# Performance work log

Hardware: AMD Instinct MI355X
Metric: run time of the kernel (lower is better)

## Reference

```python
import jax, jax.numpy as jnp
import numpy as np

B, H, W, C = 16, 64, 64, 256
DIRECTIONS = [(0, -1), (1, -1), (1, 0), (1, 1), (0, 1), (-1, 1), (-1, 0), (-1, -1)]


def _shift(g, dx, dy):
    # zero-padded shift matching the torch _shift_grid semantics:
    # result[:, max(0,dy):H+min(0,dy), max(0,dx):W+min(0,dx)] = g[src slices]
    _, h, w, _ = g.shape
    padded = jnp.pad(g, ((0, 0), (max(0, dy), max(0, -dy)), (max(0, dx), max(0, -dx)), (0, 0)))
    return padded[:, max(0, -dy):max(0, -dy) + h, max(0, -dx):max(0, -dx) + w, :]


def setup_inputs() -> dict:
    key = jax.random.key(0)
    k1, k2, k3, k4 = jax.random.split(key, 4)
    grid_embedding = jax.random.normal(k1, (B, H, W, C), dtype=jnp.float32)
    Wd = jax.random.normal(k2, (8, C, C), dtype=jnp.float32) * 0.01  # per-direction weights
    Wc = jax.random.normal(k3, (C, 8 * C), dtype=jnp.float32) * 0.02  # Linear weight [out, in]
    bc = jax.random.normal(k4, (C,), dtype=jnp.float32) * 0.02
    return {"grid_embedding": grid_embedding, "Wd": Wd, "Wc": Wc, "bc": bc}


def reference(grid_embedding, Wd, Wc, bc):
    # stack the 8 zero-padded shifted copies: [8, B, H, W, C]
    shifted = jnp.stack([_shift(grid_embedding, dx, dy) for (dx, dy) in DIRECTIONS], axis=0)
    # per-direction channel matmul: [B, H, W, 8, C] (d-major over last two dims matches torch.cat order)
    proc = jnp.einsum('dbhwc,dce->bhwde', shifted, Wd)
    combined = proc.reshape(grid_embedding.shape[0], grid_embedding.shape[1], grid_embedding.shape[2], -1)
    # nn.Linear: y = x @ W.T + b
    return combined @ Wc.T + bc
```

## Files before the change

kernel.cpp:

```cpp
#include <hip/hip_runtime.h>


typedef unsigned short u16;
typedef unsigned int u32;
typedef __attribute__((ext_vector_type(8))) short bf16x8;
typedef __attribute__((ext_vector_type(4))) float f32x4;

#define GP_BYTES 35684352

__device__ __forceinline__ u16 f2bf(float f) {
  u32 u = __float_as_uint(f);
  u32 r = u + 0x7fffu + ((u >> 16) & 1u);
  return (u16)(r >> 16);
}
__device__ __forceinline__ u32 pack2(float a, float b) {
  return (u32)f2bf(a) | ((u32)f2bf(b) << 16);
}

__global__ __launch_bounds__(256) void pad_convert(const float* __restrict__ g,
                                                   u16* __restrict__ gp) {
  int id = blockIdx.x * 256 + threadIdx.x;
  if (id >= 2230272) return;
  int c8 = id & 31;
  int t = id >> 5;
  int xx = t % 66;
  int s = t / 66;
  int yy = s % 66;
  int b  = s / 66;
  u32 o0 = 0, o1 = 0, o2 = 0, o3 = 0;
  if (yy != 0 && yy != 65 && xx != 0 && xx != 65) {
    const float* src = g + ((((b << 6) + yy - 1) << 6) + xx - 1) * 256 + (c8 << 3);
    float4 fa = *(const float4*)src;
    float4 fb = *(const float4*)(src + 4);
    o0 = pack2(fa.x, fa.y);
    o1 = pack2(fa.z, fa.w);
    o2 = pack2(fb.x, fb.y);
    o3 = pack2(fb.z, fb.w);
  }
  uint4 v; v.x = o0; v.y = o1; v.z = o2; v.w = o3;
  *(uint4*)(gp + (size_t)id * 8) = v;
}

__global__ __launch_bounds__(256) void build_mt(const float* __restrict__ Wd,
                                                const float* __restrict__ Wc,
                                                u16* __restrict__ Bf) {
  __shared__ __align__(16) u16 As[128 * 32];
  __shared__ __align__(16) u16 Bs[128 * 32];
  const int bid = blockIdx.x;
  const int n0    = (bid & 1) << 7;
  const int mblk  = bid >> 1;
  const int d     = mblk >> 1;
  const int chalf = (mblk & 1) << 7;
  const int tid  = threadIdx.x;
  const int lane = tid & 63, wid = tid >> 6;
  const int wm = (wid >> 1) << 6, wn = (wid & 1) << 6;
  const int quad = lane >> 4, r16 = lane & 15;
  const int srow = tid >> 1, hh = tid & 1;
  const int swz  = (srow >> 1) & 3;
  const int ssl  = (quad ^ ((r16 >> 1) & 3)) << 3;
  f32x4 acc[4][4] = {};

  for (int e0 = 0; e0 < 256; e0 += 32) {
    __syncthreads();
    const float* pa = Wd + (size_t)(d * 256 + chalf + srow) * 256 + e0 + hh * 16;
    const float* pb = Wc + (size_t)(n0 + srow) * 2048 + d * 256 + e0 + hh * 16;
#pragma unroll
    for (int i = 0; i < 2; ++i) {
      float4 a0 = *(const float4*)(pa + i * 8);
      float4 a1 = *(const float4*)(pa + i * 8 + 4);
      float4 b0 = *(const float4*)(pb + i * 8);
      float4 b1 = *(const float4*)(pb + i * 8 + 4);
      uint4 va, vb;
      va.x = pack2(a0.x, a0.y); va.y = pack2(a0.z, a0.w);
      va.z = pack2(a1.x, a1.y); va.w = pack2(a1.z, a1.w);
      vb.x = pack2(b0.x, b0.y); vb.y = pack2(b0.z, b0.w);
      vb.z = pack2(b1.x, b1.y); vb.w = pack2(b1.z, b1.w);
      int slot = (2 * hh + i) ^ swz;
      *(uint4*)&As[srow * 32 + slot * 8] = va;
      *(uint4*)&Bs[srow * 32 + slot * 8] = vb;
    }
    __syncthreads();
    bf16x8 bfr[4];
#pragma unroll
    for (int nt = 0; nt < 4; ++nt)
      bfr[nt] = *(const bf16x8*)&Bs[(wn + nt * 16 + r16) * 32 + ssl];
#pragma unroll
    for (int mt = 0; mt < 4; ++mt) {
      bf16x8 af = *(const bf16x8*)&As[(wm + mt * 16 + r16) * 32 + ssl];
#pragma unroll
      for (int nt = 0; nt < 4; ++nt)
        acc[mt][nt] = __builtin_amdgcn_mfma_f32_16x16x32_bf16(af, bfr[nt], acc[mt][nt], 0, 0, 0);
    }
  }
#pragma unroll
  for (int mt = 0; mt < 4; ++mt) {
#pragma unroll
    for (int nt = 0; nt < 4; ++nt) {
      const int o = n0 + wn + nt * 16 + r16;
      f32x4 v = acc[mt][nt];
#pragma unroll
      for (int r = 0; r < 4; ++r) {
        const int c = chalf + wm + mt * 16 + quad * 4 + r;
        const int lane2 = (o & 15) + (((c >> 3) & 3) << 4);
        const size_t idx = ((size_t)((d * 8 + (c >> 5)) * 16 + (o >> 4)) * 512) + lane2 * 8 + (c & 7);
        Bf[idx] = f2bf(v[r]);
      }
    }
  }
}

__constant__ int DOFF[8] = {16896, 16640, -256, -17152, -16896, -16640, 256, 17152};

__device__ __forceinline__ void async16(const u16* g, u16* l) {
  __builtin_amdgcn_global_load_lds((const __attribute__((address_space(1))) u32*)g,
                                   (__attribute__((address_space(3))) u32*)l, 16, 0, 0);
}

__global__ __launch_bounds__(512, 2) void conv_gemm(const u16* __restrict__ gp,
                                                    const u16* __restrict__ Bf,
                                                    const float* __restrict__ bc,
                                                    float* __restrict__ out) {
  __shared__ __align__(16) u16 Asm[4][8192];
  const int bid = blockIdx.x;
  const int id2 = ((bid & 7) << 5) | (bid >> 3);
  const int b   = id2 >> 4;
  const int y0  = (id2 & 15) << 2;

  const int tid  = threadIdx.x;
  const int lane = tid & 63;
  const int wid  = tid >> 6;
  const int wm   = (wid >> 2) << 7;
  const int wn   = (wid & 3) << 6;
  const int quad = lane >> 4;
  const int r16  = lane & 15;

  const int chunk = (tid & 3) ^ ((tid >> 3) & 3);
  const u16* baseA = gp + ((b * 66 + y0 + 1 + (tid >> 8)) * 66 + ((tid >> 2) & 63) + 1) * 256
                        + (chunk << 3);
  const int ldso = tid * 8;

  const u16* baseBf = Bf + ((wn >> 4) << 9) + lane * 8;

  const int ssl = (quad ^ ((r16 >> 1) & 3)) << 3;

  f32x4 acc[8][4] = {};
  bf16x8 Be[4], Bo[4];
  bf16x8 afl[4], afh[4];

  auto issueA = [&](int kt) {
    const int off = DOFF[kt >> 3] + ((kt & 7) << 5);
    async16(baseA + off,         Asm[kt & 3] + ldso);
    async16(baseA + off + 33792, Asm[kt & 3] + 4096 + ldso);
  };
  auto loadB = [&](int kt, bf16x8* dst) {
    const u16* bp = baseBf + (size_t)kt * 8192;
#pragma unroll
    for (int nt = 0; nt < 4; ++nt) dst[nt] = *(const bf16x8*)(bp + nt * 512);
  };
  auto readAh = [&](int kt, bf16x8* af, int h) {
    const u16* Ab = Asm[kt & 3];
#pragma unroll
    for (int mt = 0; mt < 4; ++mt)
      af[mt] = *(const bf16x8*)&Ab[(wm + (h * 4 + mt) * 16 + r16) * 32 + ssl];
  };
  auto mfma_half = [&](const bf16x8* af, const bf16x8* bb, int h) {
    __builtin_amdgcn_s_setprio(1);
#pragma unroll
    for (int mt = 0; mt < 4; ++mt)
#pragma unroll
      for (int nt = 0; nt < 4; ++nt)
        acc[h * 4 + mt][nt] =
            __builtin_amdgcn_mfma_f32_16x16x32_bf16(af[mt], bb[nt], acc[h * 4 + mt][nt], 0, 0, 0);
    __builtin_amdgcn_s_setprio(0);
  };

  auto body = [&](int kt, bf16x8* bu, bool doB, bool doA, int vm) {
    readAh(kt, afh, 1);
    mfma_half(afl, bu, 0);
    readAh(kt + 1, afl, 0);
    mfma_half(afh, bu, 1);
    if (doB) loadB(kt + 2, bu);
    if (doA) issueA(kt + 3);
    if (vm == 6)      asm volatile("s_waitcnt vmcnt(6)" ::: "memory");
    else if (vm == 4) asm volatile("s_waitcnt vmcnt(4)" ::: "memory");
    else              asm volatile("s_waitcnt vmcnt(0)" ::: "memory");
    asm volatile("s_barrier" ::: "memory");
  };

  loadB(0, Be);
  issueA(0);
  issueA(1);
  loadB(1, Bo);
  issueA(2);
  asm volatile("s_waitcnt vmcnt(6)" ::: "memory");
  asm volatile("s_barrier" ::: "memory");
  readAh(0, afl, 0);

  for (int kt = 0; kt < 60; kt += 2) {
    body(kt,     Be, true, true, 6);
    body(kt + 1, Bo, true, true, 6);
  }
  body(60, Be, true,  true,  6);
  body(61, Bo, true,  false, 4);
  body(62, Be, false, false, 0);
  readAh(63, afh, 1);
  mfma_half(afl, Bo, 0);
  mfma_half(afh, Bo, 1);

  const int pbase = (b * 64 + y0) * 64;
#pragma unroll
  for (int nt = 0; nt < 4; ++nt) {
    const int o = wn + nt * 16 + r16;
    const float bias = bc[o];
#pragma unroll
    for (int mt = 0; mt < 8; ++mt) {
      const int pr = pbase + wm + mt * 16 + quad * 4;
      f32x4 v = acc[mt][nt];
#pragma unroll
      for (int r = 0; r < 4; ++r)
        out[(size_t)(pr + r) * 256 + o] = v[r] + bias;
    }
  }
}

extern "C" void kernel_launch(void* const* d_in, const int* in_sizes, int n_in,
                              void* d_out, int out_size, void* d_ws, size_t ws_size,
                              hipStream_t stream) {
  const float* g  = (const float*)d_in[0];
  const float* Wd = (const float*)d_in[1];
  const float* Wc = (const float*)d_in[2];
  const float* bc = (const float*)d_in[3];
  float* out = (float*)d_out;
  u16* gp = (u16*)d_ws;
  u16* Bf = (u16*)((char*)d_ws + GP_BYTES);

  pad_convert<<<8712, 256, 0, stream>>>(g, gp);
  build_mt<<<32, 256, 0, stream>>>(Wd, Wc, Bf);
  conv_gemm<<<256, 512, 0, stream>>>(gp, Bf, bc, out);
}
```

Before: 190.4 us.

## Load padded halo slab once per channel chunk and reuse across all eight directions

Instead of issuing a separate async global-to-LDS copy of the shifted A tile for every (direction, channel-chunk) k-step, each block now loads one swizzled 6x66 padded slab per 32-channel chunk into a triple-buffered LDS ring. The eight directional shifts are taken as row offsets into that slab. This cuts global/L2 traffic for A by about 8x and removes most per-k-step barriers and waits, with a barrier only once per slab. In exchange it uses more LDS (3x12800 bf16), adds extra halo loads, and makes the B-prefetch schedule and vmcnt accounting more intricate.

Result: faster. 181.9 us (-4.5%).

```diff
diff --git a/kernel.cpp b/kernel.cpp
--- a/kernel.cpp
+++ b/kernel.cpp
@@ -109,8 +109,6 @@
   }
 }
 
-__constant__ int DOFF[8] = {16896, 16640, -256, -17152, -16896, -16640, 256, 17152};
-
 __device__ __forceinline__ void async16(const u16* g, u16* l) {
   __builtin_amdgcn_global_load_lds((const __attribute__((address_space(1))) u32*)g,
                                    (__attribute__((address_space(3))) u32*)l, 16, 0, 0);
@@ -120,7 +118,7 @@
                                                     const u16* __restrict__ Bf,
                                                     const float* __restrict__ bc,
                                                     float* __restrict__ out) {
-  __shared__ __align__(16) u16 Asm[4][8192];
+  __shared__ __align__(16) u16 slab[3][12800];
   const int bid = blockIdx.x;
   const int id2 = ((bid & 7) << 5) | (bid >> 3);
   const int b   = id2 >> 4;
@@ -134,34 +132,52 @@
   const int quad = lane >> 4;
   const int r16  = lane & 15;
 
-  const int chunk = (tid & 3) ^ ((tid >> 3) & 3);
-  const u16* baseA = gp + ((b * 66 + y0 + 1 + (tid >> 8)) * 66 + ((tid >> 2) & 63) + 1) * 256
-                        + (chunk << 3);
-  const int ldso = tid * 8;
+  const int i0 = tid, i1 = tid + 512, i2 = tid + 1024, i3 = 1536 + lane;
+  const u16 *p0, *p1, *p2, *p3;
+  {
+    const size_t rowb = (size_t)(b * 66 + y0) * 66;
+    int s, c;
+    s = i0 >> 2; c = (i0 & 3) ^ ((s >> 1) & 3);
+    p0 = gp + (rowb + (s / 66) * 66 + (s % 66)) * 256 + c * 8;
+    s = i1 >> 2; c = (i1 & 3) ^ ((s >> 1) & 3);
+    p1 = gp + (rowb + (s / 66) * 66 + (s % 66)) * 256 + c * 8;
+    s = i2 >> 2; c = (i2 & 3) ^ ((s >> 1) & 3);
+    p2 = gp + (rowb + (s / 66) * 66 + (s % 66)) * 256 + c * 8;
+    s = i3 >> 2; c = (i3 & 3) ^ ((s >> 1) & 3);
+    p3 = gp + (rowb + (s / 66) * 66 + (s % 66)) * 256 + c * 8;
+  }
+  const int l0 = i0 * 8, l1 = i1 * 8, l2 = i2 * 8, l3 = i3 * 8;
 
   const u16* baseBf = Bf + ((wn >> 4) << 9) + lane * 8;
 
-  const int ssl = (quad ^ ((r16 >> 1) & 3)) << 3;
+  const int swm = (wm >> 6) * 66 + r16;
+  const int q8  = quad << 3;
+
+  constexpr int KLO[8] = {133, 132, 66,  0,  1,  2,  68, 134};
+  constexpr int KHI[8] = {199, 198, 132, 66, 67, 68, 134, 200};
+  constexpr int LBO[8] = {2 * 65536, 3 * 65536, 4 * 65536, 5 * 65536,
+                          6 * 65536, 7 * 65536, 8192, 8192 + 65536};
 
   f32x4 acc[8][4] = {};
   bf16x8 Be[4], Bo[4];
   bf16x8 afl[4], afh[4];
 
-  auto issueA = [&](int kt) {
-    const int off = DOFF[kt >> 3] + ((kt & 7) << 5);
-    async16(baseA + off,         Asm[kt & 3] + ldso);
-    async16(baseA + off + 33792, Asm[kt & 3] + 4096 + ldso);
-  };
-  auto loadB = [&](int kt, bf16x8* dst) {
-    const u16* bp = baseBf + (size_t)kt * 8192;
-#pragma unroll
-    for (int nt = 0; nt < 4; ++nt) dst[nt] = *(const bf16x8*)(bp + nt * 512);
-  };
-  auto readAh = [&](int kt, bf16x8* af, int h) {
-    const u16* Ab = Asm[kt & 3];
-#pragma unroll
-    for (int mt = 0; mt < 4; ++mt)
-      af[mt] = *(const bf16x8*)&Ab[(wm + (h * 4 + mt) * 16 + r16) * 32 + ssl];
+  auto issueSlab = [&](u16* dst, int ch) {
+    async16(p0 + ch, dst + l0);
+    async16(p1 + ch, dst + l1);
+    async16(p2 + ch, dst + l2);
+    async16(p3 + ch, dst + l3);
+  };
+  auto loadB = [&](const u16* pB, int off, bf16x8* dst) {
+#pragma unroll
+    for (int nt = 0; nt < 4; ++nt) dst[nt] = *(const bf16x8*)(pB + off + nt * 512);
+  };
+  auto readAh = [&](const u16* bufR, int K, bf16x8* af) {
+    const int s  = swm + K;
+    const int sw = q8 ^ (((s >> 1) & 3) << 3);
+    const u16* p = bufR + s * 32 + sw;
+#pragma unroll
+    for (int mt = 0; mt < 4; ++mt) af[mt] = *(const bf16x8*)(p + mt * 512);
   };
   auto mfma_half = [&](const bf16x8* af, const bf16x8* bb, int h) {
     __builtin_amdgcn_s_setprio(1);
@@ -174,38 +190,44 @@
     __builtin_amdgcn_s_setprio(0);
   };
 
-  auto body = [&](int kt, bf16x8* bu, bool doB, bool doA, int vm) {
-    readAh(kt, afh, 1);
-    mfma_half(afl, bu, 0);
-    readAh(kt + 1, afl, 0);
-    mfma_half(afh, bu, 1);
-    if (doB) loadB(kt + 2, bu);
-    if (doA) issueA(kt + 3);
-    if (vm == 6)      asm volatile("s_waitcnt vmcnt(6)" ::: "memory");
-    else if (vm == 4) asm volatile("s_waitcnt vmcnt(4)" ::: "memory");
-    else              asm volatile("s_waitcnt vmcnt(0)" ::: "memory");
+  auto stage_core = [&](const u16* bufR, const u16* pB, bool tailLoads) {
+#pragma unroll
+    for (int d = 0; d < 8; ++d) {
+      bf16x8* bu = (d & 1) ? Bo : Be;
+      readAh(bufR, KHI[d], afh);
+      mfma_half(afl, bu, 0);
+      if (d < 7) readAh(bufR, KLO[d + 1], afl);
+      mfma_half(afh, bu, 1);
+      if (d < 6 || tailLoads) loadB(pB, LBO[d], bu);
+    }
+  };
+
+  issueSlab(slab[0], 0);
+  loadB(baseBf, 0, Be);
+  loadB(baseBf, 65536, Bo);
+  issueSlab(slab[1], 32);
+  asm volatile("s_waitcnt vmcnt(12)" ::: "memory");
+  asm volatile("s_barrier" ::: "memory");
+  readAh(slab[0], KLO[0], afl);
+
+  const u16* pB = baseBf;
+  u16* bR = slab[0]; u16* bN = slab[1]; u16* bT = slab[2];
+#pragma unroll 1
+  for (int cb = 0; cb < 6; ++cb) {
+    stage_core(bR, pB, true);
+    issueSlab(bT, (cb + 2) * 32);
+    asm volatile("s_waitcnt vmcnt(12)" ::: "memory");
     asm volatile("s_barrier" ::: "memory");
-  };
-
-  loadB(0, Be);
-  issueA(0);
-  issueA(1);
-  loadB(1, Bo);
-  issueA(2);
-  asm volatile("s_waitcnt vmcnt(6)" ::: "memory");
+    readAh(bN, KLO[0], afl);
+    u16* t = bR; bR = bN; bN = bT; bT = t;
+    pB += 8192;
+  }
+  stage_core(bR, pB, true);
+  asm volatile("s_waitcnt vmcnt(8)" ::: "memory");
   asm volatile("s_barrier" ::: "memory");
-  readAh(0, afl, 0);
-
-  for (int kt = 0; kt < 60; kt += 2) {
-    body(kt,     Be, true, true, 6);
-    body(kt + 1, Bo, true, true, 6);
-  }
-  body(60, Be, true,  true,  6);
-  body(61, Bo, true,  false, 4);
-  body(62, Be, false, false, 0);
-  readAh(63, afh, 1);
-  mfma_half(afl, Bo, 0);
-  mfma_half(afh, Bo, 1);
+  readAh(bN, KLO[0], afl);
+  pB += 8192;
+  stage_core(bN, pB, false);
 
   const int pbase = (b * 64 + y0) * 64;
 #pragma unroll
```
